# Optimization experiments

Measured on AMD Instinct MI355X. Metric: run time of the kernel, lower is better.

The kernel has to match this reference:

```python
import jax, jax.numpy as jnp
import numpy as np

B, D_IN, H, L, K, E, NL = 16384, 768, 1024, 128, 8192, 128, 3
CC = 0.25  # commitment cost
sg = jax.lax.stop_gradient


def _ln(x, g, b):
    # torch nn.LayerNorm, eps=1e-5
    m = jnp.mean(x, -1, keepdims=True)
    v = jnp.mean((x - m) ** 2, -1, keepdims=True)
    return (x - m) / jnp.sqrt(v + 1e-5) * g + b


def setup_inputs() -> dict:
    key = jax.random.key(0)
    ks = iter(jax.random.split(key, 32))
    def n(sh, s=0.02):
        return jax.random.normal(next(ks), sh, jnp.float32) * s
    return dict(
        x=jax.random.normal(next(ks), (B, D_IN), jnp.float32),
        eps=jax.random.normal(next(ks), (B, L), jnp.float32),
        enc_w1=n((D_IN, H)), enc_b1=jnp.zeros((H,), jnp.float32),
        enc_w2=n((H, H)), enc_b2=jnp.zeros((H,), jnp.float32),
        enc_w3=n((H, H)), enc_b3=jnp.zeros((H,), jnp.float32),
        mu_w=n((H, L)), mu_b=jnp.zeros((L,), jnp.float32),
        var_w=n((H, L)), var_b=jnp.zeros((L,), jnp.float32),
        dec_w1=n((L, H)), dec_b1=jnp.zeros((H,), jnp.float32),
        dec_w2=n((H, H)), dec_b2=jnp.zeros((H,), jnp.float32),
        dec_w3=n((H, D_IN)), dec_b3=jnp.zeros((D_IN,), jnp.float32),
        ln_g=jnp.ones((NL, L), jnp.float32),
        ln_b=jnp.zeros((NL, L), jnp.float32),
        q_in_w=n((NL, L, E)), q_in_b=jnp.zeros((NL, E), jnp.float32),
        codebook=jax.random.uniform(next(ks), (NL, K, E), jnp.float32,
                                    -1.0 / K, 1.0 / K),
        q_out_w=n((NL, E, L)), q_out_b=jnp.zeros((NL, L), jnp.float32),
    )


def reference(x, eps, enc_w1, enc_b1, enc_w2, enc_b2, enc_w3, enc_b3,
              mu_w, mu_b, var_w, var_b,
              dec_w1, dec_b1, dec_w2, dec_b2, dec_w3, dec_b3,
              ln_g, ln_b, q_in_w, q_in_b, codebook, q_out_w, q_out_b):
    # encoder MLP
    h = jax.nn.relu(x @ enc_w1 + enc_b1)
    h = jax.nn.relu(h @ enc_w2 + enc_b2)
    h = h @ enc_w3 + enc_b3
    mu = h @ mu_w + mu_b
    log_var = h @ var_w + var_b
    z = mu + eps * jnp.exp(0.5 * log_var)  # reparameterize

    # residual quantization over NL layers
    cur = z
    quantized = jnp.zeros_like(z)
    total_loss = jnp.float32(0.0)
    for i in range(NL):  # small fixed layer count
        nr = _ln(cur, ln_g[i], ln_b[i])                  # [B, L]
        f = nr @ q_in_w[i] + q_in_b[i]                   # [B, E]
        cb = codebook[i]                                 # [K, E]
        d = (jnp.sum(f * f, axis=1, keepdims=True)
             + jnp.sum(cb * cb, axis=1)
             - 2.0 * f @ cb.T)                           # [B, K]
        idx = jnp.argmin(d, axis=1)                      # [B]
        q = cb[idx] @ q_out_w[i] + q_out_b[i]            # gather == onehot@cb
        e_loss = jnp.mean((sg(q) - nr) ** 2)
        q_loss = jnp.mean((q - sg(nr)) ** 2)
        total_loss = total_loss + q_loss + CC * e_loss
        q_st = nr + sg(q - nr)                           # straight-through
        quantized = quantized + q_st
        cur = cur - q_st

    # decoder MLP
    r = jax.nn.relu(quantized @ dec_w1 + dec_b1)
    r = jax.nn.relu(r @ dec_w2 + dec_b2)
    recon = r @ dec_w3 + dec_b3
    return recon, mu, log_var, total_loss
```

## Files before the change

### kernel.cpp

```cpp
#include <hip/hip_runtime.h>
#include <stdint.h>


typedef float   floatx4  __attribute__((ext_vector_type(4)));
typedef __bf16  bf16x8   __attribute__((ext_vector_type(8)));
typedef unsigned short ushort4v __attribute__((ext_vector_type(4)));
typedef unsigned short bfbits;

#define AS1 __attribute__((address_space(1)))
#define AS3 __attribute__((address_space(3)))

__device__ __forceinline__ bfbits f2bf(float f) {
  unsigned u = __float_as_uint(f);
  u += 0x7fffu + ((u >> 16) & 1u);
  return (bfbits)(u >> 16);
}

__device__ __forceinline__ void load_lds16(const void* g, void* l) {
  __builtin_amdgcn_global_load_lds((AS1 void*)g, (AS3 void*)l, 16, 0, 0);
}

__global__ __launch_bounds__(256) void cvt_bf16_kernel(
    const float* __restrict__ in, bfbits* __restrict__ out, long n4) {
  long i = (long)blockIdx.x * 256 + threadIdx.x;
  if (i >= n4) return;
  float4 v = ((const float4*)in)[i];
  ushort4v o = { f2bf(v.x), f2bf(v.y), f2bf(v.z), f2bf(v.w) };
  ((ushort4v*)out)[i] = o;
}

__global__ __launch_bounds__(256) void transpose_bf16_kernel(
    const float* __restrict__ W, bfbits* __restrict__ Wt, int K, int N) {
  __shared__ float t[32][33];
  const long base = (long)blockIdx.z * K * N;
  const int k0 = blockIdx.y * 32, n0 = blockIdx.x * 32;
  const int tx = threadIdx.x & 31, ty = threadIdx.x >> 5;
#pragma unroll
  for (int j = 0; j < 32; j += 8)
    t[ty + j][tx] = W[base + (long)(k0 + ty + j) * N + n0 + tx];
  __syncthreads();
#pragma unroll
  for (int j = 0; j < 32; j += 8)
    Wt[base + (long)(n0 + ty + j) * K + k0 + tx] = f2bf(t[tx][ty + j]);
}

__global__ __launch_bounds__(256) void rownorm_kernel(
    const float* __restrict__ cb, float* __restrict__ out) {
  const int wave = threadIdx.x >> 6, lane = threadIdx.x & 63;
  const long row = (long)blockIdx.x * 4 + wave;
  const float* r = cb + row * 128;
  float a = r[lane], b = r[lane + 64];
  float s = a * a + b * b;
#pragma unroll
  for (int off = 1; off < 64; off <<= 1) s += __shfl_xor(s, off);
  if (lane == 0) out[row] = s;
}

template <bool RELU, bool OUTF32, bool DUAL>
__global__ __launch_bounds__(256) void gemm_kernel(
    const bfbits* __restrict__ A, const bfbits* __restrict__ Bt,
    const float* __restrict__ bias, bfbits* __restrict__ Cb,
    float* __restrict__ Cf, float* __restrict__ Cf2, int N, int Kd) {
  __shared__ bfbits Als[128 * 32];
  __shared__ bfbits Bls[128 * 32];
  const int tid = threadIdx.x;
  const int wave = tid >> 6, lane = tid & 63;
  const int wr = wave >> 1, wc = wave & 1;
  const int row0 = blockIdx.y << 7, col0 = blockIdx.x << 7;
  const int l15 = lane & 15, l16 = lane >> 4;
  const int srow = lane >> 2;
  const int schunk = (lane & 3) * 8;

  floatx4 acc[4][4] = {};

  for (int k0 = 0; k0 < Kd; k0 += 32) {
    __syncthreads();
#pragma unroll
    for (int j = 0; j < 2; ++j) {
      const int rb = wave * 2 + j;
      const int r = rb * 16 + srow;
      load_lds16(A + (long)(row0 + r) * Kd + (k0 + schunk),
                 Als + rb * 512 + lane * 8);
      load_lds16(Bt + (long)(col0 + r) * Kd + (k0 + schunk),
                 Bls + rb * 512 + lane * 8);
    }
    __syncthreads();
    bf16x8 af[4], bf[4];
#pragma unroll
    for (int t = 0; t < 4; ++t) {
      af[t] = *(const bf16x8*)(Als + (wr * 64 + t * 16 + l15) * 32 + l16 * 8);
      bf[t] = *(const bf16x8*)(Bls + (wc * 64 + t * 16 + l15) * 32 + l16 * 8);
    }
#pragma unroll
    for (int i = 0; i < 4; ++i)
#pragma unroll
      for (int jn = 0; jn < 4; ++jn)
        acc[i][jn] = __builtin_amdgcn_mfma_f32_16x16x32_bf16(
            af[i], bf[jn], acc[i][jn], 0, 0, 0);
  }

#pragma unroll
  for (int mt = 0; mt < 4; ++mt) {
#pragma unroll
    for (int nt = 0; nt < 4; ++nt) {
      const int col = col0 + wc * 64 + nt * 16 + l15;
      const float bv = bias[col];
      const int rowb = row0 + wr * 64 + mt * 16 + l16 * 4;
#pragma unroll
      for (int r = 0; r < 4; ++r) {
        float v = acc[mt][nt][r] + bv;
        if (RELU) v = fmaxf(v, 0.f);
        if (DUAL) {
          if (col < 128) Cf[(long)(rowb + r) * 128 + col] = v;
          else           Cf2[(long)(rowb + r) * 128 + col - 128] = v;
        } else {
          const long idx = (long)(rowb + r) * N + col;
          if (OUTF32) Cf[idx] = v; else Cb[idx] = f2bf(v);
        }
      }
    }
  }
}

__global__ __launch_bounds__(512, 2) void dist2_kernel(
    const bfbits* __restrict__ A,
    const bfbits* __restrict__ Bt,
    const float* __restrict__ cbnorm,
    int2* __restrict__ cand) {
  __shared__ alignas(16) bfbits Bls[2][128 * 128];
  const int tid = threadIdx.x;
  const int wave = tid >> 6, lane = tid & 63;
  const int wr = wave & 3, wc = wave >> 2;
  const int l15 = lane & 15, l16 = lane >> 4;
  const int row0 = blockIdx.y * 256;
  const int col0 = blockIdx.x * 2048;

  bf16x8 af[4][4];
#pragma unroll
  for (int mt = 0; mt < 4; ++mt)
#pragma unroll
    for (int s = 0; s < 4; ++s)
      af[mt][s] = *(const bf16x8*)(A + (long)(row0 + wr * 64 + mt * 16 + l15) * 128 +
                                   s * 32 + l16 * 8);

  auto stage = [&](int t, int p) {
    const bfbits* src = Bt + (long)(col0 + t * 128) * 128;
    bfbits* dst = &Bls[p][0];
#pragma unroll
    for (int q = 0; q < 4; ++q) {
      const int j = q * 512 + tid;
      const int c = j >> 4;
      const int g = (j & 15) ^ (c & 15);
      load_lds16(src + (long)c * 128 + g * 8, dst + (size_t)j * 8);
    }
  };

  stage(0, 0);

  float run_val[4][4];
  int   run_col[4][4];
#pragma unroll
  for (int mt = 0; mt < 4; ++mt)
#pragma unroll
    for (int r = 0; r < 4; ++r) { run_val[mt][r] = 3.0e38f; run_col[mt][r] = 0; }

  __syncthreads();

  for (int t = 0; t < 16; ++t) {
    const bfbits* buf = &Bls[t & 1][0];
    if (t + 1 < 16) stage(t + 1, (t + 1) & 1);

    float cn[4];
    int   colv[4];
#pragma unroll
    for (int nt = 0; nt < 4; ++nt) {
      const int cl = wc * 64 + nt * 16 + l15;
      cn[nt] = cbnorm[col0 + t * 128 + cl];
      colv[nt] = t * 128 + cl;
    }

    floatx4 acc[4][4] = {};
#pragma unroll
    for (int s = 0; s < 4; ++s) {
      bf16x8 bf[4];
#pragma unroll
      for (int nt = 0; nt < 4; ++nt) {
        const int cl = wc * 64 + nt * 16 + l15;
        bf[nt] = *(const bf16x8*)(buf + (size_t)cl * 128 +
                                  (size_t)(((s * 4 + l16) ^ l15)) * 8);
      }
#pragma unroll
      for (int mt = 0; mt < 4; ++mt)
#pragma unroll
        for (int nt = 0; nt < 4; ++nt)
          acc[mt][nt] = __builtin_amdgcn_mfma_f32_16x16x32_bf16(
              af[mt][s], bf[nt], acc[mt][nt], 0, 0, 0);
    }

#pragma unroll
    for (int mt = 0; mt < 4; ++mt)
#pragma unroll
      for (int nt = 0; nt < 4; ++nt)
#pragma unroll
        for (int r = 0; r < 4; ++r) {
          const float sc = fmaf(-2.0f, acc[mt][nt][r], cn[nt]);
          if (sc < run_val[mt][r]) { run_val[mt][r] = sc; run_col[mt][r] = colv[nt]; }
        }

    __syncthreads();
  }

#pragma unroll
  for (int mt = 0; mt < 4; ++mt)
#pragma unroll
    for (int r = 0; r < 4; ++r) {
      float v = run_val[mt][r];
      int   c = run_col[mt][r];
#pragma unroll
      for (int off = 1; off < 16; off <<= 1) {
        const float ov = __shfl_xor(v, off);
        const int   oc = __shfl_xor(c, off);
        if (ov < v || (ov == v && oc < c)) { v = ov; c = oc; }
      }
      if (l15 == 0) {
        const int row = row0 + wr * 64 + mt * 16 + l16 * 4 + r;
        cand[(long)row * 8 + blockIdx.x * 2 + wc] =
            make_int2(__float_as_int(v), col0 + c);
      }
    }
}

__global__ __launch_bounds__(256) void argmin8_kernel(
    const int2* __restrict__ cand, const float* __restrict__ cb,
    bfbits* __restrict__ cbg) {
  const int wave = threadIdx.x >> 6, lane = threadIdx.x & 63;
  const long row = (long)blockIdx.x * 4 + wave;
  float v = 3.0e38f; int k = 0x7fffffff;
  if (lane < 8) {
    int2 c = cand[row * 8 + lane];
    v = __int_as_float(c.x); k = c.y;
  }
#pragma unroll
  for (int off = 1; off < 8; off <<= 1) {
    float ov = __shfl_xor(v, off);
    int   ok = __shfl_xor(k, off);
    if (ov < v || (ov == v && ok < k)) { v = ov; k = ok; }
  }
  k = __shfl(k, 0);
  const float* src = cb + (long)k * 128;
  cbg[row * 128 + lane]      = f2bf(src[lane]);
  cbg[row * 128 + lane + 64] = f2bf(src[lane + 64]);
}

__device__ __forceinline__ void ln_row(float c0, float c1, int lane,
                                       const float* __restrict__ g,
                                       const float* __restrict__ bta,
                                       long row, bfbits* __restrict__ nrb,
                                       float* __restrict__ nrf) {
  float s = c0 + c1, sq = c0 * c0 + c1 * c1;
#pragma unroll
  for (int off = 1; off < 64; off <<= 1) {
    s += __shfl_xor(s, off);
    sq += __shfl_xor(sq, off);
  }
  const float m = s * (1.f / 128.f);
  const float var = fmaxf(sq * (1.f / 128.f) - m * m, 0.f);
  const float rstd = rsqrtf(var + 1e-5f);
  const float y0 = (c0 - m) * rstd * g[lane] + bta[lane];
  const float y1 = (c1 - m) * rstd * g[lane + 64] + bta[lane + 64];
  nrf[row * 128 + lane] = y0;
  nrf[row * 128 + lane + 64] = y1;
  nrb[row * 128 + lane] = f2bf(y0);
  nrb[row * 128 + lane + 64] = f2bf(y1);
}

__global__ __launch_bounds__(256) void reparam_ln_kernel(
    const float* __restrict__ mu, const float* __restrict__ lv,
    const float* __restrict__ eps, float* __restrict__ cur,
    float* __restrict__ qnt, const float* __restrict__ g,
    const float* __restrict__ bta, bfbits* __restrict__ nrb,
    float* __restrict__ nrf) {
  const int wave = threadIdx.x >> 6, lane = threadIdx.x & 63;
  const long row = (long)blockIdx.x * 4 + wave;
  const long i0 = row * 128 + lane, i1 = i0 + 64;
  const float z0 = mu[i0] + eps[i0] * expf(0.5f * lv[i0]);
  const float z1 = mu[i1] + eps[i1] * expf(0.5f * lv[i1]);
  cur[i0] = z0; cur[i1] = z1;
  qnt[i0] = 0.f; qnt[i1] = 0.f;
  ln_row(z0, z1, lane, g, bta, row, nrb, nrf);
}

template <bool DO_LN>
__global__ __launch_bounds__(256) void qupd_ln_kernel(
    const float* __restrict__ q, float* __restrict__ nrf,
    float* __restrict__ cur, float* __restrict__ qnt,
    const float* __restrict__ g, const float* __restrict__ bta,
    bfbits* __restrict__ nrb, float* __restrict__ lossp) {
  const int wave = threadIdx.x >> 6, lane = threadIdx.x & 63;
  const long row = (long)blockIdx.x * 4 + wave;
  const long i0 = row * 128 + lane, i1 = i0 + 64;
  const float q0 = q[i0], q1 = q[i1];
  const float d0 = q0 - nrf[i0], d1 = q1 - nrf[i1];
  qnt[i0] += q0; qnt[i1] += q1;
  float p = d0 * d0 + d1 * d1;
#pragma unroll
  for (int off = 1; off < 64; off <<= 1) p += __shfl_xor(p, off);
  __shared__ float sp[4];
  if (lane == 0) sp[wave] = p;
  __syncthreads();
  if (threadIdx.x == 0) lossp[blockIdx.x] = sp[0] + sp[1] + sp[2] + sp[3];
  if (DO_LN) {
    const float c0 = cur[i0] - q0, c1 = cur[i1] - q1;
    cur[i0] = c0; cur[i1] = c1;
    ln_row(c0, c1, lane, g, bta, row, nrb, nrf);
  }
}

__global__ __launch_bounds__(256) void loss_reduce_kernel(
    const float* __restrict__ lossp, float* __restrict__ out, int n) {
  float s = 0.f;
  for (int i = threadIdx.x; i < n; i += 256) s += lossp[i];
#pragma unroll
  for (int off = 1; off < 64; off <<= 1) s += __shfl_xor(s, off);
  __shared__ float sp[4];
  const int wave = threadIdx.x >> 6, lane = threadIdx.x & 63;
  if (lane == 0) sp[wave] = s;
  __syncthreads();
  if (threadIdx.x == 0)
    *out = (sp[0] + sp[1] + sp[2] + sp[3]) * (1.25f / 2097152.f);
}

static void launch_gemm(bool relu, bool outf32, const bfbits* A,
                        const bfbits* Bt, const float* bias, bfbits* Cb,
                        float* Cf, int M, int N, int Kd, hipStream_t s) {
  dim3 g(N / 128, M / 128), b(256);
  if (relu) {
    gemm_kernel<true, false, false><<<g, b, 0, s>>>(A, Bt, bias, Cb, Cf, nullptr, N, Kd);
  } else if (outf32) {
    gemm_kernel<false, true, false><<<g, b, 0, s>>>(A, Bt, bias, Cb, Cf, nullptr, N, Kd);
  } else {
    gemm_kernel<false, false, false><<<g, b, 0, s>>>(A, Bt, bias, Cb, Cf, nullptr, N, Kd);
  }
}

extern "C" void kernel_launch(void* const* d_in, const int* in_sizes, int n_in,
                              void* d_out, int out_size, void* d_ws,
                              size_t ws_size, hipStream_t stream) {
  (void)in_sizes; (void)n_in; (void)out_size; (void)ws_size;
  constexpr long B = 16384, DIN = 768, H = 1024, L = 128, K = 8192;

  const float* x    = (const float*)d_in[0];
  const float* eps  = (const float*)d_in[1];
  const float* ew1  = (const float*)d_in[2];
  const float* eb1  = (const float*)d_in[3];
  const float* ew2  = (const float*)d_in[4];
  const float* eb2  = (const float*)d_in[5];
  const float* ew3  = (const float*)d_in[6];
  const float* eb3  = (const float*)d_in[7];
  const float* muw  = (const float*)d_in[8];
  const float* mub  = (const float*)d_in[9];
  const float* vaw  = (const float*)d_in[10];
  const float* vab  = (const float*)d_in[11];
  const float* dw1  = (const float*)d_in[12];
  const float* db1  = (const float*)d_in[13];
  const float* dw2  = (const float*)d_in[14];
  const float* db2  = (const float*)d_in[15];
  const float* dw3  = (const float*)d_in[16];
  const float* db3  = (const float*)d_in[17];
  const float* lng  = (const float*)d_in[18];
  const float* lnb  = (const float*)d_in[19];
  const float* qinw = (const float*)d_in[20];
  const float* qinb = (const float*)d_in[21];
  const float* cb   = (const float*)d_in[22];
  const float* qow  = (const float*)d_in[23];
  const float* qob  = (const float*)d_in[24];

  float* out = (float*)d_out;
  float* out_mu   = out + B * DIN;
  float* out_lv   = out_mu + B * L;
  float* out_loss = out_lv + B * L;

  char* ws = (char*)d_ws;
  constexpr size_t O_W1T  = 0;
  constexpr size_t O_W2T  = O_W1T + 1024 * 768 * 2;
  constexpr size_t O_W3T  = O_W2T + 1024 * 1024 * 2;
  constexpr size_t O_MUT  = O_W3T + 1024 * 1024 * 2;
  constexpr size_t O_VART = O_MUT + 128 * 1024 * 2;
  constexpr size_t O_DW1T = O_VART + 128 * 1024 * 2;
  constexpr size_t O_DW2T = O_DW1T + 1024 * 128 * 2;
  constexpr size_t O_DW3T = O_DW2T + 1024 * 1024 * 2;
  constexpr size_t O_QINT = O_DW3T + 768 * 1024 * 2;
  constexpr size_t O_QOUT = O_QINT + 3 * 128 * 128 * 2;
  constexpr size_t O_CBB  = O_QOUT + 3 * 128 * 128 * 2;
  constexpr size_t O_CBN  = O_CBB + 3 * 8192 * 128 * 2;
  constexpr size_t O_B2   = O_CBN + 3 * 8192 * 4;
  constexpr size_t O_LOSSP= O_B2 + 256 * 4;
  constexpr size_t O_CUR  = O_LOSSP + 3 * 4096 * 4;
  constexpr size_t O_QNT  = O_CUR + B * L * 4;
  constexpr size_t O_NRF  = O_QNT + B * L * 4;
  constexpr size_t O_H1   = O_NRF + B * L * 4;
  constexpr size_t O_H2   = O_H1 + B * H * 2;
  constexpr size_t O_H3   = O_H2 + B * H * 2;
  constexpr size_t O_NRB  = O_H2;
  constexpr size_t O_FB   = O_H2 + B * L * 2;
  constexpr size_t O_CBG  = O_H2 + 2 * B * L * 2;
  constexpr size_t O_QBUF = O_H2 + 3 * B * L * 2;
  constexpr size_t O_CAND = O_H2 + 3 * B * L * 2 + B * L * 4;
  constexpr size_t O_XB   = O_H3;
  constexpr size_t O_QZB  = O_H3;

  bfbits* w1t  = (bfbits*)(ws + O_W1T);
  bfbits* w2t  = (bfbits*)(ws + O_W2T);
  bfbits* w3t  = (bfbits*)(ws + O_W3T);
  bfbits* mut  = (bfbits*)(ws + O_MUT);
  bfbits* vart = (bfbits*)(ws + O_VART);
  bfbits* dw1t = (bfbits*)(ws + O_DW1T);
  bfbits* dw2t = (bfbits*)(ws + O_DW2T);
  bfbits* dw3t = (bfbits*)(ws + O_DW3T);
  bfbits* qint = (bfbits*)(ws + O_QINT);
  bfbits* qout = (bfbits*)(ws + O_QOUT);
  bfbits* cbb  = (bfbits*)(ws + O_CBB);
  float*  cbn  = (float*)(ws + O_CBN);
  float*  bias2= (float*)(ws + O_B2);
  float*  lossp= (float*)(ws + O_LOSSP);
  float*  cur  = (float*)(ws + O_CUR);
  float*  qnt  = (float*)(ws + O_QNT);
  float*  nrf  = (float*)(ws + O_NRF);
  bfbits* h1   = (bfbits*)(ws + O_H1);
  bfbits* h2   = (bfbits*)(ws + O_H2);
  bfbits* h3   = (bfbits*)(ws + O_H3);
  bfbits* nrb  = (bfbits*)(ws + O_NRB);
  bfbits* fb   = (bfbits*)(ws + O_FB);
  bfbits* cbg  = (bfbits*)(ws + O_CBG);
  float*  qbuf = (float*)(ws + O_QBUF);
  int2*   cand = (int2*)(ws + O_CAND);
  bfbits* xb   = (bfbits*)(ws + O_XB);
  bfbits* qzb  = (bfbits*)(ws + O_QZB);
  bfbits* r1   = h1;
  bfbits* r2   = h2;

  cvt_bf16_kernel<<<dim3((B * DIN) / 4 / 256), dim3(256), 0, stream>>>(x, xb, (B * DIN) / 4);
  cvt_bf16_kernel<<<dim3((3 * K * 128) / 4 / 256), dim3(256), 0, stream>>>(cb, cbb, (3 * K * 128) / 4);
  transpose_bf16_kernel<<<dim3(1024 / 32, 768 / 32, 1), dim3(256), 0, stream>>>(ew1, w1t, 768, 1024);
  transpose_bf16_kernel<<<dim3(32, 32, 1), dim3(256), 0, stream>>>(ew2, w2t, 1024, 1024);
  transpose_bf16_kernel<<<dim3(32, 32, 1), dim3(256), 0, stream>>>(ew3, w3t, 1024, 1024);
  transpose_bf16_kernel<<<dim3(128 / 32, 32, 1), dim3(256), 0, stream>>>(muw, mut, 1024, 128);
  transpose_bf16_kernel<<<dim3(128 / 32, 32, 1), dim3(256), 0, stream>>>(vaw, vart, 1024, 128);
  transpose_bf16_kernel<<<dim3(32, 128 / 32, 1), dim3(256), 0, stream>>>(dw1, dw1t, 128, 1024);
  transpose_bf16_kernel<<<dim3(32, 32, 1), dim3(256), 0, stream>>>(dw2, dw2t, 1024, 1024);
  transpose_bf16_kernel<<<dim3(768 / 32, 32, 1), dim3(256), 0, stream>>>(dw3, dw3t, 1024, 768);
  transpose_bf16_kernel<<<dim3(4, 4, 3), dim3(256), 0, stream>>>(qinw, qint, 128, 128);
  transpose_bf16_kernel<<<dim3(4, 4, 3), dim3(256), 0, stream>>>(qow, qout, 128, 128);
  rownorm_kernel<<<dim3(3 * K / 4), dim3(256), 0, stream>>>(cb, cbn);
  hipMemcpyAsync(bias2, mub, 128 * 4, hipMemcpyDeviceToDevice, stream);
  hipMemcpyAsync(bias2 + 128, vab, 128 * 4, hipMemcpyDeviceToDevice, stream);

  launch_gemm(true, false, xb, w1t, eb1, h1, nullptr, B, 1024, 768, stream);
  launch_gemm(true, false, h1, w2t, eb2, h2, nullptr, B, 1024, 1024, stream);
  launch_gemm(false, false, h2, w3t, eb3, h3, nullptr, B, 1024, 1024, stream);
  gemm_kernel<false, true, true><<<dim3(2, 128), dim3(256), 0, stream>>>(
      h3, mut, bias2, nullptr, out_mu, out_lv, 256, 1024);

  reparam_ln_kernel<<<dim3(B / 4), dim3(256), 0, stream>>>(
      out_mu, out_lv, eps, cur, qnt, lng, lnb, nrb, nrf);

  for (int i = 0; i < 3; ++i) {
    launch_gemm(false, false, nrb, qint + (size_t)i * 128 * 128,
                qinb + i * 128, fb, nullptr, B, 128, 128, stream);
    dist2_kernel<<<dim3(4, 64), dim3(512), 0, stream>>>(
        fb, cbb + (size_t)i * K * 128, cbn + (size_t)i * K, cand);
    argmin8_kernel<<<dim3(B / 4), dim3(256), 0, stream>>>(
        cand, cb + (size_t)i * K * 128, cbg);
    launch_gemm(false, true, cbg, qout + (size_t)i * 128 * 128,
                qob + i * 128, nullptr, qbuf, B, 128, 128, stream);
    if (i < 2) {
      qupd_ln_kernel<true><<<dim3(B / 4), dim3(256), 0, stream>>>(
          qbuf, nrf, cur, qnt, lng + (i + 1) * 128, lnb + (i + 1) * 128,
          nrb, lossp + (size_t)i * 4096);
    } else {
      qupd_ln_kernel<false><<<dim3(B / 4), dim3(256), 0, stream>>>(
          qbuf, nrf, cur, qnt, nullptr, nullptr, nullptr,
          lossp + (size_t)i * 4096);
    }
  }
  loss_reduce_kernel<<<dim3(1), dim3(256), 0, stream>>>(lossp, out_loss, 3 * 4096);

  cvt_bf16_kernel<<<dim3((B * L) / 4 / 256), dim3(256), 0, stream>>>(qnt, qzb, (B * L) / 4);
  launch_gemm(true, false, qzb, dw1t, db1, r1, nullptr, B, 1024, 128, stream);
  launch_gemm(true, false, r1, dw2t, db2, r2, nullptr, B, 1024, 1024, stream);
  launch_gemm(false, true, r2, dw3t, db3, nullptr, out, B, 768, 1024, stream);
}
```

Measured before the change: 758.6 us.

## Deepen GEMM K-tile to 64 with XOR-swizzled LDS and add 64-row N=128 GEMM

The generic bf16 MFMA GEMM now stages 64-wide K slices instead of 32. This halves the number of barrier-separated load/compute iterations, and the LDS layout uses an XOR swizzle to avoid bank conflicts on fragment reads. The grid is reordered so blockIdx.x walks rows. A new N=128 specialised kernel with 64-row tiles replaces the quantizer in/out projections, giving more blocks for those small GEMMs. LDS use per block doubles, which may reduce occupancy.

```diff
diff --git a/kernel.cpp b/kernel.cpp
--- a/kernel.cpp
+++ b/kernel.cpp
@@ -61,42 +61,47 @@
     const bfbits* __restrict__ A, const bfbits* __restrict__ Bt,
     const float* __restrict__ bias, bfbits* __restrict__ Cb,
     float* __restrict__ Cf, float* __restrict__ Cf2, int N, int Kd) {
-  __shared__ bfbits Als[128 * 32];
-  __shared__ bfbits Bls[128 * 32];
+  __shared__ bfbits Als[128 * 64];
+  __shared__ bfbits Bls[128 * 64];
   const int tid = threadIdx.x;
   const int wave = tid >> 6, lane = tid & 63;
   const int wr = wave >> 1, wc = wave & 1;
-  const int row0 = blockIdx.y << 7, col0 = blockIdx.x << 7;
+  const int row0 = blockIdx.x << 7, col0 = blockIdx.y << 7;
   const int l15 = lane & 15, l16 = lane >> 4;
-  const int srow = lane >> 2;
-  const int schunk = (lane & 3) * 8;
+  const int jrow = lane >> 3;
+  const int gchunk = (lane & 7) ^ jrow;
 
   floatx4 acc[4][4] = {};
 
-  for (int k0 = 0; k0 < Kd; k0 += 32) {
+  for (int k0 = 0; k0 < Kd; k0 += 64) {
     __syncthreads();
 #pragma unroll
-    for (int j = 0; j < 2; ++j) {
-      const int rb = wave * 2 + j;
-      const int r = rb * 16 + srow;
-      load_lds16(A + (long)(row0 + r) * Kd + (k0 + schunk),
-                 Als + rb * 512 + lane * 8);
-      load_lds16(Bt + (long)(col0 + r) * Kd + (k0 + schunk),
-                 Bls + rb * 512 + lane * 8);
+    for (int j = 0; j < 4; ++j) {
+      const int gi = wave * 4 + j;
+      const int r = gi * 8 + jrow;
+      load_lds16(A + (long)(row0 + r) * Kd + (k0 + gchunk * 8),
+                 Als + gi * 512 + lane * 8);
+      load_lds16(Bt + (long)(col0 + r) * Kd + (k0 + gchunk * 8),
+                 Bls + gi * 512 + lane * 8);
     }
     __syncthreads();
-    bf16x8 af[4], bf[4];
-#pragma unroll
-    for (int t = 0; t < 4; ++t) {
-      af[t] = *(const bf16x8*)(Als + (wr * 64 + t * 16 + l15) * 32 + l16 * 8);
-      bf[t] = *(const bf16x8*)(Bls + (wc * 64 + t * 16 + l15) * 32 + l16 * 8);
-    }
-#pragma unroll
-    for (int i = 0; i < 4; ++i)
-#pragma unroll
-      for (int jn = 0; jn < 4; ++jn)
-        acc[i][jn] = __builtin_amdgcn_mfma_f32_16x16x32_bf16(
-            af[i], bf[jn], acc[i][jn], 0, 0, 0);
+#pragma unroll
+    for (int kk = 0; kk < 2; ++kk) {
+      bf16x8 af[4], bf[4];
+#pragma unroll
+      for (int t = 0; t < 4; ++t) {
+        const int ar = wr * 64 + t * 16 + l15;
+        af[t] = *(const bf16x8*)(Als + ar * 64 + (((kk * 4 + l16) ^ (ar & 7)) * 8));
+        const int br = wc * 64 + t * 16 + l15;
+        bf[t] = *(const bf16x8*)(Bls + br * 64 + (((kk * 4 + l16) ^ (br & 7)) * 8));
+      }
+#pragma unroll
+      for (int i = 0; i < 4; ++i)
+#pragma unroll
+        for (int jn = 0; jn < 4; ++jn)
+          acc[i][jn] = __builtin_amdgcn_mfma_f32_16x16x32_bf16(
+              af[i], bf[jn], acc[i][jn], 0, 0, 0);
+    }
   }
 
 #pragma unroll
@@ -117,6 +122,81 @@
           const long idx = (long)(rowb + r) * N + col;
           if (OUTF32) Cf[idx] = v; else Cb[idx] = f2bf(v);
         }
+      }
+    }
+  }
+}
+
+template <bool OUTF32>
+__global__ __launch_bounds__(256) void gemm_n128_kernel(
+    const bfbits* __restrict__ A, const bfbits* __restrict__ Bt,
+    const float* __restrict__ bias, bfbits* __restrict__ Cb,
+    float* __restrict__ Cf) {
+  __shared__ bfbits Als[64 * 64];
+  __shared__ bfbits Bls[128 * 64];
+  const int tid = threadIdx.x;
+  const int wave = tid >> 6, lane = tid & 63;
+  const int wr = wave >> 1, wc = wave & 1;
+  const int row0 = blockIdx.x << 6;
+  const int l15 = lane & 15, l16 = lane >> 4;
+  const int jrow = lane >> 3;
+  const int gchunk = (lane & 7) ^ jrow;
+
+  floatx4 acc[2][4] = {};
+
+  for (int k0 = 0; k0 < 128; k0 += 64) {
+    __syncthreads();
+    {
+#pragma unroll
+      for (int j = 0; j < 2; ++j) {
+        const int gi = wave * 2 + j;
+        const int r = gi * 8 + jrow;
+        load_lds16(A + (long)(row0 + r) * 128 + (k0 + gchunk * 8),
+                   Als + gi * 512 + lane * 8);
+      }
+#pragma unroll
+      for (int j = 0; j < 4; ++j) {
+        const int gi = wave * 4 + j;
+        const int r = gi * 8 + jrow;
+        load_lds16(Bt + (long)r * 128 + (k0 + gchunk * 8),
+                   Bls + gi * 512 + lane * 8);
+      }
+    }
+    __syncthreads();
+#pragma unroll
+    for (int kk = 0; kk < 2; ++kk) {
+      bf16x8 af[2], bf[4];
+#pragma unroll
+      for (int t = 0; t < 2; ++t) {
+        const int ar = wr * 32 + t * 16 + l15;
+        af[t] = *(const bf16x8*)(Als + ar * 64 + (((kk * 4 + l16) ^ (ar & 7)) * 8));
+      }
+#pragma unroll
+      for (int t = 0; t < 4; ++t) {
+        const int br = wc * 64 + t * 16 + l15;
+        bf[t] = *(const bf16x8*)(Bls + br * 64 + (((kk * 4 + l16) ^ (br & 7)) * 8));
+      }
+#pragma unroll
+      for (int i = 0; i < 2; ++i)
+#pragma unroll
+        for (int jn = 0; jn < 4; ++jn)
+          acc[i][jn] = __builtin_amdgcn_mfma_f32_16x16x32_bf16(
+              af[i], bf[jn], acc[i][jn], 0, 0, 0);
+    }
+  }
+
+#pragma unroll
+  for (int mt = 0; mt < 2; ++mt) {
+#pragma unroll
+    for (int nt = 0; nt < 4; ++nt) {
+      const int col = wc * 64 + nt * 16 + l15;
+      const float bv = bias[col];
+      const int rowb = row0 + wr * 32 + mt * 16 + l16 * 4;
+#pragma unroll
+      for (int r = 0; r < 4; ++r) {
+        const float v = acc[mt][nt][r] + bv;
+        const long idx = (long)(rowb + r) * 128 + col;
+        if (OUTF32) Cf[idx] = v; else Cb[idx] = f2bf(v);
       }
     }
   }
@@ -333,7 +413,7 @@
 static void launch_gemm(bool relu, bool outf32, const bfbits* A,
                         const bfbits* Bt, const float* bias, bfbits* Cb,
                         float* Cf, int M, int N, int Kd, hipStream_t s) {
-  dim3 g(N / 128, M / 128), b(256);
+  dim3 g(M / 128, N / 128), b(256);
   if (relu) {
     gemm_kernel<true, false, false><<<g, b, 0, s>>>(A, Bt, bias, Cb, Cf, nullptr, N, Kd);
   } else if (outf32) {
@@ -458,21 +538,21 @@
   launch_gemm(true, false, xb, w1t, eb1, h1, nullptr, B, 1024, 768, stream);
   launch_gemm(true, false, h1, w2t, eb2, h2, nullptr, B, 1024, 1024, stream);
   launch_gemm(false, false, h2, w3t, eb3, h3, nullptr, B, 1024, 1024, stream);
-  gemm_kernel<false, true, true><<<dim3(2, 128), dim3(256), 0, stream>>>(
+  gemm_kernel<false, true, true><<<dim3(128, 2), dim3(256), 0, stream>>>(
       h3, mut, bias2, nullptr, out_mu, out_lv, 256, 1024);
 
   reparam_ln_kernel<<<dim3(B / 4), dim3(256), 0, stream>>>(
       out_mu, out_lv, eps, cur, qnt, lng, lnb, nrb, nrf);
 
   for (int i = 0; i < 3; ++i) {
-    launch_gemm(false, false, nrb, qint + (size_t)i * 128 * 128,
-                qinb + i * 128, fb, nullptr, B, 128, 128, stream);
+    gemm_n128_kernel<false><<<dim3(B / 64), dim3(256), 0, stream>>>(
+        nrb, qint + (size_t)i * 128 * 128, qinb + i * 128, fb, nullptr);
     dist2_kernel<<<dim3(4, 64), dim3(512), 0, stream>>>(
         fb, cbb + (size_t)i * K * 128, cbn + (size_t)i * K, cand);
     argmin8_kernel<<<dim3(B / 4), dim3(256), 0, stream>>>(
         cand, cb + (size_t)i * K * 128, cbg);
-    launch_gemm(false, true, cbg, qout + (size_t)i * 128 * 128,
-                qob + i * 128, nullptr, qbuf, B, 128, 128, stream);
+    gemm_n128_kernel<true><<<dim3(B / 64), dim3(256), 0, stream>>>(
+        cbg, qout + (size_t)i * 128 * 128, qob + i * 128, nullptr, qbuf);
     if (i < 2) {
       qupd_ln_kernel<true><<<dim3(B / 4), dim3(256), 0, stream>>>(
           qbuf, nrf, cur, qnt, lng + (i + 1) * 128, lnb + (i + 1) * 128,
```

Result: faster. 662.9 us (-12.6%).
